# Kernel optimization log

Hardware: AMD Instinct MI355X
Metric: run time of the kernel (lower is better)

The kernel has to match this reference:

```python
import jax, jax.numpy as jnp
import numpy as np

B, NSV, NTRK, K, H = 512, 128, 512, 8, 16


def setup_inputs() -> dict:
    key = jax.random.key(0)
    ks = jax.random.split(key, 12)
    p = lambda k, shp: (jax.random.normal(k, shp, dtype=jnp.float32) * 0.1)
    return {
        "x_sv": jax.random.normal(ks[0], (B * NSV, 2), dtype=jnp.float32),
        "x_trk": jax.random.normal(ks[1], (B * NTRK, 8), dtype=jnp.float32),
        "batch_sv": jnp.repeat(jnp.arange(B, dtype=jnp.int32), NSV),
        "batch_trk": jnp.repeat(jnp.arange(B, dtype=jnp.int32), NTRK),
        # sv_encode: Linear(2,16) -> ELU -> Linear(16,16)
        "W1s": p(ks[2], (2, H)), "b1s": jnp.zeros((H,), jnp.float32),
        "W2s": p(ks[3], (H, H)), "b2s": jnp.zeros((H,), jnp.float32),
        # trk_encode: Linear(8,16) -> ELU -> Linear(16,16)
        "W1t": p(ks[4], (8, H)), "b1t": jnp.zeros((H,), jnp.float32),
        "W2t": p(ks[5], (H, H)), "b2t": jnp.zeros((H,), jnp.float32),
        # edge MLP: Linear(2*16, 16)
        "We": p(ks[6], (2 * H, H)), "be": jnp.zeros((H,), jnp.float32),
        # output head: Linear(16, 1)
        "Wo": p(ks[7], (H, 1)), "bo": jnp.zeros((1,), jnp.float32),
    }


def reference(x_sv, x_trk, batch_sv, batch_trk,
              W1s, b1s, W2s, b2s, W1t, b1t, W2t, b2t, We, be, Wo, bo):
    # Node encoders
    sv = jax.nn.elu(x_sv @ W1s + b1s) @ W2s + b2s      # [Nsv, H]
    trk = jax.nn.elu(x_trk @ W1t + b1t) @ W2t + b2t    # [Ntrk, H]

    # Regular batching: reshape to per-event blocks (batch_sv/batch_trk are
    # contiguous repeats of arange(B) with NSV / NTRK nodes per event).
    svb = sv.reshape(B, NSV, H)      # [B, S, H]
    trkb = trk.reshape(B, NTRK, H)   # [B, T, H]

    # kNN in encoded space: squared L2 distance per event, k nearest SVs per track
    t_sq = jnp.sum(trkb * trkb, -1)[:, :, None]          # [B, T, 1]
    s_sq = jnp.sum(svb * svb, -1)[:, None, :]            # [B, 1, S]
    dots = jnp.einsum("bth,bsh->bts", trkb, svb)         # [B, T, S]
    d2 = t_sq + s_sq - 2.0 * dots                        # [B, T, S]
    _, idx = jax.lax.top_k(-d2, K)                       # [B, T, K] indices into S

    # Gather neighbor SV features: [B, T, K, H]
    nbr = jax.vmap(lambda s, i: s[i])(svb, idx)

    # EdgeConv message: nn(cat[x_i, x_j - x_i]), x_i = track (target), x_j = SV
    ti = trkb[:, :, None, :]                                    # [B, T, 1, H]
    msg_in = jnp.concatenate(
        [jnp.broadcast_to(ti, nbr.shape), nbr - ti], axis=-1)   # [B, T, K, 2H]
    msg = msg_in @ We + be                                      # [B, T, K, H]
    feats = jnp.max(msg, axis=2).reshape(B * NTRK, H)           # max aggregation

    # Output head + per-event average pool (avg_pool_x with cluster == batch)
    out = jax.nn.sigmoid(feats @ Wo + bo)                       # [Ntrk, 1]
    sums = jax.ops.segment_sum(out, batch_trk, num_segments=B)  # [B, 1]
    cnts = jax.ops.segment_sum(jnp.ones_like(out), batch_trk, num_segments=B)
    pooled = sums / cnts                                        # [B, 1]
    batch_out = jnp.arange(B, dtype=jnp.int32)
    return pooled, batch_out
```

## Files before the change

### kernel.cpp

```cpp
#include <hip/hip_runtime.h>
#include <cmath>

#define BB   512
#define NSV  128
#define NTRK 512
#define KK   8
#define HH   16
#define TPB  512
#define TST  40
#define SST  24
#define PSTR 20

typedef float f32x4  __attribute__((ext_vector_type(4)));
typedef short bf16x8 __attribute__((ext_vector_type(8)));

__device__ __forceinline__ float elu_f(float x) {
    float e = __builtin_amdgcn_exp2f(x * 1.44269504088896341f) - 1.0f;
    return x > 0.0f ? x : e;
}
__device__ __forceinline__ unsigned umin_u(unsigned a, unsigned b) { return a < b ? a : b; }
__device__ __forceinline__ unsigned umax_u(unsigned a, unsigned b) { return a > b ? a : b; }
__device__ __forceinline__ unsigned med3u(unsigned a, unsigned b, unsigned c) {
    unsigned d;
    asm("v_med3_u32 %0, %1, %2, %3" : "=v"(d) : "v"(a), "v"(b), "v"(c));
    return d;
}

__global__ __launch_bounds__(TPB, 4) void fused_all(
    const float* __restrict__ x_sv, const float* __restrict__ x_trk,
    const float* __restrict__ W1s, const float* __restrict__ b1s,
    const float* __restrict__ W2s, const float* __restrict__ b2s,
    const float* __restrict__ W1t, const float* __restrict__ b1t,
    const float* __restrict__ W2t, const float* __restrict__ b2t,
    const float* __restrict__ We,  const float* __restrict__ be,
    const float* __restrict__ Wo,  const float* __restrict__ bo,
    float* __restrict__ out)
{
    __shared__ __align__(16) short    Tsh[NTRK * TST];
    __shared__ __align__(16) short    ShiS[NSV * SST];
    __shared__ __align__(16) short    SloS[NSV * SST];
    __shared__ __align__(16) float    hsqS[NSV];
    __shared__ __align__(16) float    proj[NSV][PSTR];
    __shared__ __align__(16) unsigned knnS[NTRK * KK];
    __shared__ float ucS[HH + 1];
    __shared__ float sred[TPB / 64];

    const int b   = blockIdx.x, tid = threadIdx.x;

    {
        const float* xp = x_trk + (size_t)(b * NTRK + tid) * 8;
        float x[8];
        *(float4*)&x[0] = *(const float4*)&xp[0];
        *(float4*)&x[4] = *(const float4*)&xp[4];
        float hb[HH];
        #pragma unroll
        for (int h = 0; h < HH; ++h) {
            float a = b1t[h];
            #pragma unroll
            for (int i = 0; i < 8; ++i) a += x[i] * W1t[i * HH + h];
            hb[h] = elu_f(a);
        }
        float tf[HH], sq = 0.0f;
        #pragma unroll
        for (int h2 = 0; h2 < HH; ++h2) {
            float a = b2t[h2];
            #pragma unroll
            for (int h = 0; h < HH; ++h) a += hb[h] * W2t[h * HH + h2];
            tf[h2] = a;
            sq += a * a;
        }
        unsigned hw[8], lw[8];
        #pragma unroll
        for (int j = 0; j < 8; ++j) {
            float f0 = tf[2 * j], f1 = tf[2 * j + 1];
            unsigned u0 = __float_as_uint(f0) & 0xFFFF0000u;
            unsigned u1 = __float_as_uint(f1) & 0xFFFF0000u;
            hw[j] = (u0 >> 16) | u1;
            float r0 = f0 - __uint_as_float(u0);
            float r1 = f1 - __uint_as_float(u1);
            lw[j] = (__float_as_uint(r0) >> 16) | (__float_as_uint(r1) & 0xFFFF0000u);
        }
        short* tr = &Tsh[tid * TST];
        *(uint4*)(tr + 0)  = make_uint4(hw[0], hw[1], hw[2], hw[3]);
        *(uint4*)(tr + 8)  = make_uint4(hw[4], hw[5], hw[6], hw[7]);
        *(uint4*)(tr + 16) = make_uint4(lw[0], lw[1], lw[2], lw[3]);
        *(uint4*)(tr + 24) = make_uint4(lw[4], lw[5], lw[6], lw[7]);
        *(float*)(tr + 32) = 0.5f * sq;
    }

    if (tid < NSV) {
        const float* xp = x_sv + (size_t)(b * NSV + tid) * 2;
        float x0 = xp[0], x1 = xp[1];
        float hb[HH];
        #pragma unroll
        for (int h = 0; h < HH; ++h)
            hb[h] = elu_f(x0 * W1s[h] + x1 * W1s[HH + h] + b1s[h]);
        float o[HH], sq = 0.0f;
        #pragma unroll
        for (int h2 = 0; h2 < HH; ++h2) {
            float a = b2s[h2];
            #pragma unroll
            for (int h = 0; h < HH; ++h) a += hb[h] * W2s[h * HH + h2];
            o[h2] = a;
            sq += a * a;
        }
        unsigned hw[8], lw[8];
        #pragma unroll
        for (int j = 0; j < 8; ++j) {
            float f0 = o[2 * j], f1 = o[2 * j + 1];
            unsigned u0 = __float_as_uint(f0) & 0xFFFF0000u;
            unsigned u1 = __float_as_uint(f1) & 0xFFFF0000u;
            hw[j] = (u0 >> 16) | u1;
            float r0 = f0 - __uint_as_float(u0);
            float r1 = f1 - __uint_as_float(u1);
            lw[j] = (__float_as_uint(r0) >> 16) | (__float_as_uint(r1) & 0xFFFF0000u);
        }
        short* sh = &ShiS[tid * SST];
        short* sl = &SloS[tid * SST];
        *(uint4*)(sh + 0) = make_uint4(hw[0], hw[1], hw[2], hw[3]);
        *(uint4*)(sh + 8) = make_uint4(hw[4], hw[5], hw[6], hw[7]);
        *(uint4*)(sl + 0) = make_uint4(lw[0], lw[1], lw[2], lw[3]);
        *(uint4*)(sl + 8) = make_uint4(lw[4], lw[5], lw[6], lw[7]);
        hsqS[tid] = 0.5f * sq;
        #pragma unroll
        for (int h = 0; h < HH; ++h) {
            float a = 0.0f;
            #pragma unroll
            for (int j = 0; j < HH; ++j) a += o[j] * We[(HH + j) * HH + h];
            proj[tid][h] = a;
        }
    } else if (tid < NSV + HH) {
        int j = tid - NSV;
        float a = 0.0f;
        #pragma unroll
        for (int h = 0; h < HH; ++h)
            a += (We[j * HH + h] - We[(HH + j) * HH + h]) * Wo[h];
        ucS[j] = a;
    } else if (tid == NSV + HH) {
        float a = bo[0];
        #pragma unroll
        for (int h = 0; h < HH; ++h) a += be[h] * Wo[h];
        ucS[HH] = a;
    }

    __syncthreads();

    {
        const int lane = tid & 63;
        const int w    = tid >> 6;
        const int c    = lane & 15;
        const int g    = lane >> 4;
        const int g4   = g << 2;
        const int gk   = g << 3;
        const int gah  = (g & 1) << 3;

        #pragma unroll
        for (int i = 0; i < 4; ++i) {
            const int tt  = w + 8 * i;
            const int trk = tt * 16 + c;
            const short* tb = &Tsh[trk * TST];
            bf16x8 bfrag = *(const bf16x8*)(tb + gk);
            float  htsq  = *(const float*)(tb + 32);

            f32x4 acc[8];
            #pragma unroll
            for (int ss = 0; ss < 8; ++ss) acc[ss] = (f32x4){0.f, 0.f, 0.f, 0.f};
            #pragma unroll
            for (int ss = 0; ss < 8; ++ss) {
                const int svr = ss * 16 + c;
                bf16x8 a1 = *(const bf16x8*)&ShiS[svr * SST + gah];
                bf16x8 a2 = *(const bf16x8*)&SloS[svr * SST + gah];
                acc[ss] = __builtin_amdgcn_mfma_f32_16x16x32_bf16(a1, bfrag, acc[ss], 0, 0, 0);
                acc[ss] = __builtin_amdgcn_mfma_f32_16x16x32_bf16(a2, bfrag, acc[ss], 0, 0, 0);
            }

            unsigned k0 = ~0u, k1 = ~0u, k2 = ~0u, k3 = ~0u,
                     k4 = ~0u, k5 = ~0u, k6 = ~0u, k7 = ~0u;
            #define CHAIN(v)                                               \
                do {                                                       \
                    unsigned nk0 = umin_u(v, k0);                          \
                    unsigned nk1 = med3u(v, k0, k1);                       \
                    unsigned nk2 = med3u(v, k1, k2);                       \
                    unsigned nk3 = med3u(v, k2, k3);                       \
                    unsigned nk4 = med3u(v, k3, k4);                       \
                    unsigned nk5 = med3u(v, k4, k5);                       \
                    unsigned nk6 = med3u(v, k5, k6);                       \
                    unsigned nk7 = med3u(v, k6, k7);                       \
                    k0 = nk0; k1 = nk1; k2 = nk2; k3 = nk3;                \
                    k4 = nk4; k5 = nk5; k6 = nk6; k7 = nk7;                \
                } while (0)
            #pragma unroll
            for (int ss = 0; ss < 8; ++ss) {
                f32x4 hq = *(const f32x4*)&hsqS[ss * 16 + g4];
                float e0 = fmaxf((htsq + hq.x) - acc[ss].x, 0.0f);
                float e1 = fmaxf((htsq + hq.y) - acc[ss].y, 0.0f);
                float e2 = fmaxf((htsq + hq.z) - acc[ss].z, 0.0f);
                float e3 = fmaxf((htsq + hq.w) - acc[ss].w, 0.0f);
                unsigned v0 = (__float_as_uint(e0) & 0xFFFFFF80u) | (unsigned)(g4 + ss * 16 + 0);
                CHAIN(v0);
                unsigned v1 = (__float_as_uint(e1) & 0xFFFFFF80u) | (unsigned)(g4 + ss * 16 + 1);
                CHAIN(v1);
                unsigned v2 = (__float_as_uint(e2) & 0xFFFFFF80u) | (unsigned)(g4 + ss * 16 + 2);
                CHAIN(v2);
                unsigned v3 = (__float_as_uint(e3) & 0xFFFFFF80u) | (unsigned)(g4 + ss * 16 + 3);
                CHAIN(v3);
            }
            #undef CHAIN

            unsigned m0 = umin_u(k0, __shfl_xor(k7, 32, 64));
            unsigned m1 = umin_u(k1, __shfl_xor(k6, 32, 64));
            unsigned m2 = umin_u(k2, __shfl_xor(k5, 32, 64));
            unsigned m3 = umin_u(k3, __shfl_xor(k4, 32, 64));
            unsigned m4 = umin_u(k4, __shfl_xor(k3, 32, 64));
            unsigned m5 = umin_u(k5, __shfl_xor(k2, 32, 64));
            unsigned m6 = umin_u(k6, __shfl_xor(k1, 32, 64));
            unsigned m7 = umin_u(k7, __shfl_xor(k0, 32, 64));
            #define CEX(a, bq) do { unsigned _lo = umin_u(a, bq); unsigned _hi = umax_u(a, bq); a = _lo; bq = _hi; } while (0)
            CEX(m0, m4); CEX(m1, m5); CEX(m2, m6); CEX(m3, m7);
            CEX(m0, m2); CEX(m1, m3); CEX(m4, m6); CEX(m5, m7);
            CEX(m0, m1); CEX(m2, m3); CEX(m4, m5); CEX(m6, m7);
            #undef CEX
            unsigned f0 = umin_u(m0, __shfl_xor(m7, 16, 64));
            unsigned f1 = umin_u(m1, __shfl_xor(m6, 16, 64));
            unsigned f2 = umin_u(m2, __shfl_xor(m5, 16, 64));
            unsigned f3 = umin_u(m3, __shfl_xor(m4, 16, 64));
            unsigned f4 = umin_u(m4, __shfl_xor(m3, 16, 64));
            unsigned f5 = umin_u(m5, __shfl_xor(m2, 16, 64));
            unsigned f6 = umin_u(m6, __shfl_xor(m1, 16, 64));
            unsigned f7 = umin_u(m7, __shfl_xor(m0, 16, 64));
            if (g == 0) {
                *(uint4*)&knnS[trk * KK]     = make_uint4(f0, f1, f2, f3);
                *(uint4*)&knnS[trk * KK + 4] = make_uint4(f4, f5, f6, f7);
            }
        }
    }

    __syncthreads();

    float local;
    {
        const short* tr = &Tsh[tid * TST];
        uint4 ha = *(const uint4*)(tr + 0);
        uint4 hbq = *(const uint4*)(tr + 8);
        uint4 la = *(const uint4*)(tr + 16);
        uint4 lb = *(const uint4*)(tr + 24);
        unsigned hwv[8] = {ha.x, ha.y, ha.z, ha.w, hbq.x, hbq.y, hbq.z, hbq.w};
        unsigned lwv[8] = {la.x, la.y, la.z, la.w, lb.x, lb.y, lb.z, lb.w};
        float tf[HH];
        #pragma unroll
        for (int j = 0; j < 8; ++j) {
            tf[2 * j]     = __uint_as_float(hwv[j] << 16) + __uint_as_float(lwv[j] << 16);
            tf[2 * j + 1] = __uint_as_float(hwv[j] & 0xFFFF0000u) + __uint_as_float(lwv[j] & 0xFFFF0000u);
        }
        float acc = ucS[HH];
        #pragma unroll
        for (int h = 0; h < HH; ++h) acc = fmaf(tf[h], ucS[h], acc);

        uint4 ka = *(const uint4*)&knnS[tid * KK];
        uint4 kb = *(const uint4*)&knnS[tid * KK + 4];
        unsigned idx[KK] = {ka.x, ka.y, ka.z, ka.w, kb.x, kb.y, kb.z, kb.w};
        float mx[HH];
        #pragma unroll
        for (int h = 0; h < HH; ++h) mx[h] = -INFINITY;
        #pragma unroll
        for (int q = 0; q < KK; ++q) {
            const float* pr = &proj[idx[q] & 127u][0];
            #pragma unroll
            for (int h4 = 0; h4 < 4; ++h4) {
                float4 p = *(const float4*)&pr[h4 * 4];
                mx[h4 * 4 + 0] = fmaxf(mx[h4 * 4 + 0], p.x);
                mx[h4 * 4 + 1] = fmaxf(mx[h4 * 4 + 1], p.y);
                mx[h4 * 4 + 2] = fmaxf(mx[h4 * 4 + 2], p.z);
                mx[h4 * 4 + 3] = fmaxf(mx[h4 * 4 + 3], p.w);
            }
        }
        #pragma unroll
        for (int h = 0; h < HH; ++h) acc = fmaf(mx[h], Wo[h], acc);

        float t = __builtin_amdgcn_exp2f(acc * -1.44269504088896341f);
        local = __builtin_amdgcn_rcpf(1.0f + t);
    }

    #pragma unroll
    for (int off = 32; off > 0; off >>= 1)
        local += __shfl_down(local, off, 64);
    if ((tid & 63) == 0) sred[tid >> 6] = local;
    __syncthreads();
    if (tid == 0) {
        float tot = 0.0f;
        #pragma unroll
        for (int w = 0; w < TPB / 64; ++w) tot += sred[w];
        out[b]      = tot * (1.0f / NTRK);
        out[BB + b] = (float)b;
    }
}

extern "C" void kernel_launch(void* const* d_in, const int* in_sizes, int n_in,
                              void* d_out, int out_size, void* d_ws, size_t ws_size,
                              hipStream_t stream) {
    const float* x_sv  = (const float*)d_in[0];
    const float* x_trk = (const float*)d_in[1];
    const float* W1s = (const float*)d_in[4];
    const float* b1s = (const float*)d_in[5];
    const float* W2s = (const float*)d_in[6];
    const float* b2s = (const float*)d_in[7];
    const float* W1t = (const float*)d_in[8];
    const float* b1t = (const float*)d_in[9];
    const float* W2t = (const float*)d_in[10];
    const float* b2t = (const float*)d_in[11];
    const float* We  = (const float*)d_in[12];
    const float* be  = (const float*)d_in[13];
    const float* Wo  = (const float*)d_in[14];
    const float* bo  = (const float*)d_in[15];
    float* out = (float*)d_out;

    fused_all<<<BB, TPB, 0, stream>>>(x_sv, x_trk,
                                      W1s, b1s, W2s, b2s,
                                      W1t, b1t, W2t, b2t,
                                      We, be, Wo, bo,
                                      out);
}
```

Baseline: 126.4 us.

## Fuse edge aggregation into kNN loop, hoist SV fragments, repack LDS strides

The per-track output head (gather of projected SV features, max, dot with Wo, sigmoid) now runs inside the kNN loop, split across the four lane groups and combined with shuffles. This drops the knnS buffer and one block-wide barrier. SV MFMA fragments are loaded once into registers instead of being re-read per track tile. Hi and lo bf16 parts are merged into a single array with an odd-word stride of 36 to reduce LDS bank conflicts, and the MFMAs are issued in groups of four so the top-k chain can interleave with them. In exchange it holds 16 fragment registers per thread, which raises register pressure under launch bounds of 4 blocks per unit.

```diff
diff --git a/kernel.cpp b/kernel.cpp
--- a/kernel.cpp
+++ b/kernel.cpp
@@ -7,12 +7,13 @@
 #define KK   8
 #define HH   16
 #define TPB  512
-#define TST  40
-#define SST  24
+#define TST  36
+#define SST  36
 #define PSTR 20
 
-typedef float f32x4  __attribute__((ext_vector_type(4)));
-typedef short bf16x8 __attribute__((ext_vector_type(8)));
+typedef float    f32x4  __attribute__((ext_vector_type(4)));
+typedef short    bf16x8 __attribute__((ext_vector_type(8)));
+typedef unsigned u32x4  __attribute__((ext_vector_type(4)));
 
 __device__ __forceinline__ float elu_f(float x) {
     float e = __builtin_amdgcn_exp2f(x * 1.44269504088896341f) - 1.0f;
@@ -25,6 +26,11 @@
     asm("v_med3_u32 %0, %1, %2, %3" : "=v"(d) : "v"(a), "v"(b), "v"(c));
     return d;
 }
+__device__ __forceinline__ bf16x8 mk_bf8(uint2 a, uint2 b) {
+    u32x4 u; u.x = a.x; u.y = a.y; u.z = b.x; u.w = b.y;
+    return __builtin_bit_cast(bf16x8, u);
+}
+__device__ __forceinline__ float uasf(unsigned u) { return __uint_as_float(u); }
 
 __global__ __launch_bounds__(TPB, 4) void fused_all(
     const float* __restrict__ x_sv, const float* __restrict__ x_trk,
@@ -36,16 +42,15 @@
     const float* __restrict__ Wo,  const float* __restrict__ bo,
     float* __restrict__ out)
 {
-    __shared__ __align__(16) short    Tsh[NTRK * TST];
-    __shared__ __align__(16) short    ShiS[NSV * SST];
-    __shared__ __align__(16) short    SloS[NSV * SST];
-    __shared__ __align__(16) float    hsqS[NSV];
-    __shared__ __align__(16) float    proj[NSV][PSTR];
-    __shared__ __align__(16) unsigned knnS[NTRK * KK];
-    __shared__ float ucS[HH + 1];
+    __shared__ __align__(16) short Tsh[NTRK * TST];
+    __shared__ __align__(16) short Ssh[NSV * SST];
+    __shared__ __align__(16) float hsqS[NSV];
+    __shared__ __align__(16) float proj[NSV][PSTR];
+    __shared__ __align__(16) float ucS[HH + 1];
+    __shared__ __align__(16) float WoS[HH];
     __shared__ float sred[TPB / 64];
 
-    const int b   = blockIdx.x, tid = threadIdx.x;
+    const int b = blockIdx.x, tid = threadIdx.x;
 
     {
         const float* xp = x_trk + (size_t)(b * NTRK + tid) * 8;
@@ -76,16 +81,20 @@
             unsigned u0 = __float_as_uint(f0) & 0xFFFF0000u;
             unsigned u1 = __float_as_uint(f1) & 0xFFFF0000u;
             hw[j] = (u0 >> 16) | u1;
-            float r0 = f0 - __uint_as_float(u0);
-            float r1 = f1 - __uint_as_float(u1);
+            float r0 = f0 - uasf(u0);
+            float r1 = f1 - uasf(u1);
             lw[j] = (__float_as_uint(r0) >> 16) | (__float_as_uint(r1) & 0xFFFF0000u);
         }
-        short* tr = &Tsh[tid * TST];
-        *(uint4*)(tr + 0)  = make_uint4(hw[0], hw[1], hw[2], hw[3]);
-        *(uint4*)(tr + 8)  = make_uint4(hw[4], hw[5], hw[6], hw[7]);
-        *(uint4*)(tr + 16) = make_uint4(lw[0], lw[1], lw[2], lw[3]);
-        *(uint4*)(tr + 24) = make_uint4(lw[4], lw[5], lw[6], lw[7]);
-        *(float*)(tr + 32) = 0.5f * sq;
+        unsigned* tr = (unsigned*)&Tsh[tid * TST];
+        *(uint2*)(tr + 0)  = make_uint2(hw[0], hw[1]);
+        *(uint2*)(tr + 2)  = make_uint2(hw[2], hw[3]);
+        *(uint2*)(tr + 4)  = make_uint2(hw[4], hw[5]);
+        *(uint2*)(tr + 6)  = make_uint2(hw[6], hw[7]);
+        *(uint2*)(tr + 8)  = make_uint2(lw[0], lw[1]);
+        *(uint2*)(tr + 10) = make_uint2(lw[2], lw[3]);
+        *(uint2*)(tr + 12) = make_uint2(lw[4], lw[5]);
+        *(uint2*)(tr + 14) = make_uint2(lw[6], lw[7]);
+        ((float*)tr)[16] = 0.5f * sq;
     }
 
     if (tid < NSV) {
@@ -111,16 +120,19 @@
             unsigned u0 = __float_as_uint(f0) & 0xFFFF0000u;
             unsigned u1 = __float_as_uint(f1) & 0xFFFF0000u;
             hw[j] = (u0 >> 16) | u1;
-            float r0 = f0 - __uint_as_float(u0);
-            float r1 = f1 - __uint_as_float(u1);
+            float r0 = f0 - uasf(u0);
+            float r1 = f1 - uasf(u1);
             lw[j] = (__float_as_uint(r0) >> 16) | (__float_as_uint(r1) & 0xFFFF0000u);
         }
-        short* sh = &ShiS[tid * SST];
-        short* sl = &SloS[tid * SST];
-        *(uint4*)(sh + 0) = make_uint4(hw[0], hw[1], hw[2], hw[3]);
-        *(uint4*)(sh + 8) = make_uint4(hw[4], hw[5], hw[6], hw[7]);
-        *(uint4*)(sl + 0) = make_uint4(lw[0], lw[1], lw[2], lw[3]);
-        *(uint4*)(sl + 8) = make_uint4(lw[4], lw[5], lw[6], lw[7]);
+        unsigned* sr = (unsigned*)&Ssh[tid * SST];
+        *(uint2*)(sr + 0)  = make_uint2(hw[0], hw[1]);
+        *(uint2*)(sr + 2)  = make_uint2(hw[2], hw[3]);
+        *(uint2*)(sr + 4)  = make_uint2(hw[4], hw[5]);
+        *(uint2*)(sr + 6)  = make_uint2(hw[6], hw[7]);
+        *(uint2*)(sr + 8)  = make_uint2(lw[0], lw[1]);
+        *(uint2*)(sr + 10) = make_uint2(lw[2], lw[3]);
+        *(uint2*)(sr + 12) = make_uint2(lw[4], lw[5]);
+        *(uint2*)(sr + 14) = make_uint2(lw[6], lw[7]);
         hsqS[tid] = 0.5f * sq;
         #pragma unroll
         for (int h = 0; h < HH; ++h) {
@@ -136,7 +148,10 @@
         for (int h = 0; h < HH; ++h)
             a += (We[j * HH + h] - We[(HH + j) * HH + h]) * Wo[h];
         ucS[j] = a;
-    } else if (tid == NSV + HH) {
+    } else if (tid < NSV + 2 * HH) {
+        int j = tid - NSV - HH;
+        WoS[j] = Wo[j];
+    } else if (tid == NSV + 2 * HH) {
         float a = bo[0];
         #pragma unroll
         for (int h = 0; h < HH; ++h) a += be[h] * Wo[h];
@@ -145,34 +160,35 @@
 
     __syncthreads();
 
+    float wsum = 0.0f;
     {
         const int lane = tid & 63;
         const int w    = tid >> 6;
         const int c    = lane & 15;
         const int g    = lane >> 4;
         const int g4   = g << 2;
-        const int gk   = g << 3;
-        const int gah  = (g & 1) << 3;
+        const int gd   = (g & 1) << 2;
+
+        bf16x8 sfh[8], sfl[8];
+        #pragma unroll
+        for (int ss = 0; ss < 8; ++ss) {
+            const unsigned* sp = (const unsigned*)&Ssh[(ss * 16 + c) * SST];
+            uint2 h0 = *(const uint2*)(sp + gd);
+            uint2 h1 = *(const uint2*)(sp + gd + 2);
+            uint2 l0 = *(const uint2*)(sp + 8 + gd);
+            uint2 l1 = *(const uint2*)(sp + 8 + gd + 2);
+            sfh[ss] = mk_bf8(h0, h1);
+            sfl[ss] = mk_bf8(l0, l1);
+        }
 
         #pragma unroll
         for (int i = 0; i < 4; ++i) {
-            const int tt  = w + 8 * i;
-            const int trk = tt * 16 + c;
-            const short* tb = &Tsh[trk * TST];
-            bf16x8 bfrag = *(const bf16x8*)(tb + gk);
-            float  htsq  = *(const float*)(tb + 32);
-
-            f32x4 acc[8];
-            #pragma unroll
-            for (int ss = 0; ss < 8; ++ss) acc[ss] = (f32x4){0.f, 0.f, 0.f, 0.f};
-            #pragma unroll
-            for (int ss = 0; ss < 8; ++ss) {
-                const int svr = ss * 16 + c;
-                bf16x8 a1 = *(const bf16x8*)&ShiS[svr * SST + gah];
-                bf16x8 a2 = *(const bf16x8*)&SloS[svr * SST + gah];
-                acc[ss] = __builtin_amdgcn_mfma_f32_16x16x32_bf16(a1, bfrag, acc[ss], 0, 0, 0);
-                acc[ss] = __builtin_amdgcn_mfma_f32_16x16x32_bf16(a2, bfrag, acc[ss], 0, 0, 0);
-            }
+            const int trk = (w + 8 * i) * 16 + c;
+            const unsigned* tp = (const unsigned*)&Tsh[trk * TST];
+            uint2 bq0 = *(const uint2*)(tp + g * 4);
+            uint2 bq1 = *(const uint2*)(tp + g * 4 + 2);
+            bf16x8 bfrag = mk_bf8(bq0, bq1);
+            const float htsq = ((const float*)tp)[16];
 
             unsigned k0 = ~0u, k1 = ~0u, k2 = ~0u, k3 = ~0u,
                      k4 = ~0u, k5 = ~0u, k6 = ~0u, k7 = ~0u;
@@ -189,22 +205,41 @@
                     k0 = nk0; k1 = nk1; k2 = nk2; k3 = nk3;                \
                     k4 = nk4; k5 = nk5; k6 = nk6; k7 = nk7;                \
                 } while (0)
-            #pragma unroll
-            for (int ss = 0; ss < 8; ++ss) {
-                f32x4 hq = *(const f32x4*)&hsqS[ss * 16 + g4];
-                float e0 = fmaxf((htsq + hq.x) - acc[ss].x, 0.0f);
-                float e1 = fmaxf((htsq + hq.y) - acc[ss].y, 0.0f);
-                float e2 = fmaxf((htsq + hq.z) - acc[ss].z, 0.0f);
-                float e3 = fmaxf((htsq + hq.w) - acc[ss].w, 0.0f);
-                unsigned v0 = (__float_as_uint(e0) & 0xFFFFFF80u) | (unsigned)(g4 + ss * 16 + 0);
-                CHAIN(v0);
-                unsigned v1 = (__float_as_uint(e1) & 0xFFFFFF80u) | (unsigned)(g4 + ss * 16 + 1);
-                CHAIN(v1);
-                unsigned v2 = (__float_as_uint(e2) & 0xFFFFFF80u) | (unsigned)(g4 + ss * 16 + 2);
-                CHAIN(v2);
-                unsigned v3 = (__float_as_uint(e3) & 0xFFFFFF80u) | (unsigned)(g4 + ss * 16 + 3);
-                CHAIN(v3);
+            #define CONSUME(accv, ssid)                                    \
+                do {                                                       \
+                    f32x4 hq = *(const f32x4*)&hsqS[(ssid) * 16 + g4];     \
+                    float e0 = fmaxf((htsq - accv.x) + hq.x, 0.0f);        \
+                    float e1 = fmaxf((htsq - accv.y) + hq.y, 0.0f);        \
+                    float e2 = fmaxf((htsq - accv.z) + hq.z, 0.0f);        \
+                    float e3 = fmaxf((htsq - accv.w) + hq.w, 0.0f);        \
+                    unsigned v0 = (__float_as_uint(e0) & 0xFFFFFF80u) | (unsigned)((ssid) * 16 + g4 + 0); \
+                    CHAIN(v0);                                             \
+                    unsigned v1 = (__float_as_uint(e1) & 0xFFFFFF80u) | (unsigned)((ssid) * 16 + g4 + 1); \
+                    CHAIN(v1);                                             \
+                    unsigned v2 = (__float_as_uint(e2) & 0xFFFFFF80u) | (unsigned)((ssid) * 16 + g4 + 2); \
+                    CHAIN(v2);                                             \
+                    unsigned v3 = (__float_as_uint(e3) & 0xFFFFFF80u) | (unsigned)((ssid) * 16 + g4 + 3); \
+                    CHAIN(v3);                                             \
+                } while (0)
+
+            #pragma unroll
+            for (int half = 0; half < 2; ++half) {
+                const int s0 = half * 4;
+                f32x4 a0 = {0.f, 0.f, 0.f, 0.f}, a1 = a0, a2 = a0, a3 = a0;
+                a0 = __builtin_amdgcn_mfma_f32_16x16x32_bf16(sfh[s0 + 0], bfrag, a0, 0, 0, 0);
+                a1 = __builtin_amdgcn_mfma_f32_16x16x32_bf16(sfh[s0 + 1], bfrag, a1, 0, 0, 0);
+                a2 = __builtin_amdgcn_mfma_f32_16x16x32_bf16(sfh[s0 + 2], bfrag, a2, 0, 0, 0);
+                a3 = __builtin_amdgcn_mfma_f32_16x16x32_bf16(sfh[s0 + 3], bfrag, a3, 0, 0, 0);
+                a0 = __builtin_amdgcn_mfma_f32_16x16x32_bf16(sfl[s0 + 0], bfrag, a0, 0, 0, 0);
+                a1 = __builtin_amdgcn_mfma_f32_16x16x32_bf16(sfl[s0 + 1], bfrag, a1, 0, 0, 0);
+                a2 = __builtin_amdgcn_mfma_f32_16x16x32_bf16(sfl[s0 + 2], bfrag, a2, 0, 0, 0);
+                a3 = __builtin_amdgcn_mfma_f32_16x16x32_bf16(sfl[s0 + 3], bfrag, a3, 0, 0, 0);
+                CONSUME(a0, s0 + 0);
+                CONSUME(a1, s0 + 1);
+                CONSUME(a2, s0 + 2);
+                CONSUME(a3, s0 + 3);
             }
+            #undef CONSUME
             #undef CHAIN
 
             unsigned m0 = umin_u(k0, __shfl_xor(k7, 32, 64));
@@ -228,68 +263,49 @@
             unsigned f5 = umin_u(m5, __shfl_xor(m2, 16, 64));
             unsigned f6 = umin_u(m6, __shfl_xor(m1, 16, 64));
             unsigned f7 = umin_u(m7, __shfl_xor(m0, 16, 64));
-            if (g == 0) {
-                *(uint4*)&knnS[trk * KK]     = make_uint4(f0, f1, f2, f3);
-                *(uint4*)&knnS[trk * KK + 4] = make_uint4(f4, f5, f6, f7);
-            }
-        }
-    }
-
-    __syncthreads();
-
-    float local;
-    {
-        const short* tr = &Tsh[tid * TST];
-        uint4 ha = *(const uint4*)(tr + 0);
-        uint4 hbq = *(const uint4*)(tr + 8);
-        uint4 la = *(const uint4*)(tr + 16);
-        uint4 lb = *(const uint4*)(tr + 24);
-        unsigned hwv[8] = {ha.x, ha.y, ha.z, ha.w, hbq.x, hbq.y, hbq.z, hbq.w};
-        unsigned lwv[8] = {la.x, la.y, la.z, la.w, lb.x, lb.y, lb.z, lb.w};
-        float tf[HH];
-        #pragma unroll
-        for (int j = 0; j < 8; ++j) {
-            tf[2 * j]     = __uint_as_float(hwv[j] << 16) + __uint_as_float(lwv[j] << 16);
-            tf[2 * j + 1] = __uint_as_float(hwv[j] & 0xFFFF0000u) + __uint_as_float(lwv[j] & 0xFFFF0000u);
-        }
-        float acc = ucS[HH];
-        #pragma unroll
-        for (int h = 0; h < HH; ++h) acc = fmaf(tf[h], ucS[h], acc);
-
-        uint4 ka = *(const uint4*)&knnS[tid * KK];
-        uint4 kb = *(const uint4*)&knnS[tid * KK + 4];
-        unsigned idx[KK] = {ka.x, ka.y, ka.z, ka.w, kb.x, kb.y, kb.z, kb.w};
-        float mx[HH];
-        #pragma unroll
-        for (int h = 0; h < HH; ++h) mx[h] = -INFINITY;
-        #pragma unroll
-        for (int q = 0; q < KK; ++q) {
-            const float* pr = &proj[idx[q] & 127u][0];
-            #pragma unroll
-            for (int h4 = 0; h4 < 4; ++h4) {
-                float4 p = *(const float4*)&pr[h4 * 4];
-                mx[h4 * 4 + 0] = fmaxf(mx[h4 * 4 + 0], p.x);
-                mx[h4 * 4 + 1] = fmaxf(mx[h4 * 4 + 1], p.y);
-                mx[h4 * 4 + 2] = fmaxf(mx[h4 * 4 + 2], p.z);
-                mx[h4 * 4 + 3] = fmaxf(mx[h4 * 4 + 3], p.w);
-            }
-        }
-        #pragma unroll
-        for (int h = 0; h < HH; ++h) acc = fmaf(mx[h], Wo[h], acc);
-
-        float t = __builtin_amdgcn_exp2f(acc * -1.44269504088896341f);
-        local = __builtin_amdgcn_rcpf(1.0f + t);
+
+            uint2 th = *(const uint2*)(tp + 2 * g);
+            uint2 tl = *(const uint2*)(tp + 8 + 2 * g);
+            float tfa = uasf(th.x << 16)         + uasf(tl.x << 16);
+            float tfb = uasf(th.x & 0xFFFF0000u) + uasf(tl.x & 0xFFFF0000u);
+            float tfc = uasf(th.y << 16)         + uasf(tl.y << 16);
+            float tfd = uasf(th.y & 0xFFFF0000u) + uasf(tl.y & 0xFFFF0000u);
+            f32x4 uc4 = *(const f32x4*)&ucS[g4];
+            f32x4 wo4 = *(const f32x4*)&WoS[g4];
+            float part = (g == 0) ? ucS[HH] : 0.0f;
+            part = fmaf(tfa, uc4.x, part);
+            part = fmaf(tfb, uc4.y, part);
+            part = fmaf(tfc, uc4.z, part);
+            part = fmaf(tfd, uc4.w, part);
+            f32x4 mx = {-INFINITY, -INFINITY, -INFINITY, -INFINITY};
+            mx = __builtin_elementwise_max(mx, *(const f32x4*)&proj[f0 & 127u][g4]);
+            mx = __builtin_elementwise_max(mx, *(const f32x4*)&proj[f1 & 127u][g4]);
+            mx = __builtin_elementwise_max(mx, *(const f32x4*)&proj[f2 & 127u][g4]);
+            mx = __builtin_elementwise_max(mx, *(const f32x4*)&proj[f3 & 127u][g4]);
+            mx = __builtin_elementwise_max(mx, *(const f32x4*)&proj[f4 & 127u][g4]);
+            mx = __builtin_elementwise_max(mx, *(const f32x4*)&proj[f5 & 127u][g4]);
+            mx = __builtin_elementwise_max(mx, *(const f32x4*)&proj[f6 & 127u][g4]);
+            mx = __builtin_elementwise_max(mx, *(const f32x4*)&proj[f7 & 127u][g4]);
+            part = fmaf(mx.x, wo4.x, part);
+            part = fmaf(mx.y, wo4.y, part);
+            part = fmaf(mx.z, wo4.z, part);
+            part = fmaf(mx.w, wo4.w, part);
+            part += __shfl_xor(part, 16, 64);
+            part += __shfl_xor(part, 32, 64);
+            float sg = __builtin_amdgcn_rcpf(1.0f + __builtin_amdgcn_exp2f(part * -1.44269504088896341f));
+            if (g == 0) wsum += sg;
+        }
     }
 
     #pragma unroll
     for (int off = 32; off > 0; off >>= 1)
-        local += __shfl_down(local, off, 64);
-    if ((tid & 63) == 0) sred[tid >> 6] = local;
+        wsum += __shfl_down(wsum, off, 64);
+    if ((tid & 63) == 0) sred[tid >> 6] = wsum;
     __syncthreads();
     if (tid == 0) {
         float tot = 0.0f;
         #pragma unroll
-        for (int w = 0; w < TPB / 64; ++w) tot += sred[w];
+        for (int w2 = 0; w2 < TPB / 64; ++w2) tot += sred[w2];
         out[b]      = tot * (1.0f / NTRK);
         out[BB + b] = (float)b;
     }
```

Result: slower. 138.1 us (+9.3%).
